# Kernel tuning notes

Hardware: AMD Instinct MI355X
Metric: run time of the kernel (lower is better)

The kernel has to match this reference:

```python
import jax, jax.numpy as jnp
import numpy as np

EPS = 1e-5  # torch LayerNorm default

def ln(x, g, b):
    m = jnp.mean(x, axis=-1, keepdims=True)
    v = jnp.var(x, axis=-1, keepdims=True)
    return (x - m) / jnp.sqrt(v + EPS) * g + b

def setup_inputs() -> dict:
    key = jax.random.key(0)
    H, B, L = 1024, 8, 2048
    ks = jax.random.split(key, 4)
    s = 0.02
    f32 = jnp.float32
    return {
        "x_seq": jax.random.normal(ks[0], (B, L, H), f32),
        "h_prev": jnp.zeros((B, H), f32),
        "w_z": (jax.random.normal(ks[1], (H, 2 * H), f32) * s),
        "b_z": jnp.zeros((H,), f32),
        "w_r": (jax.random.normal(ks[2], (H, 2 * H), f32) * s),
        "b_r": jnp.zeros((H,), f32),
        "w_h": (jax.random.normal(ks[3], (H, 2 * H), f32) * s),
        "b_h": jnp.zeros((H,), f32),
        "g_in": jnp.ones((H,), f32), "b_in": jnp.zeros((H,), f32),
        "g_st": jnp.ones((H,), f32), "b_st": jnp.zeros((H,), f32),
        "g_out": jnp.ones((H,), f32), "b_out": jnp.zeros((H,), f32),
    }

def reference(x_seq, h_prev, w_z, b_z, w_r, b_r, w_h, b_h,
              g_in, b_in, g_st, b_st, g_out, b_out):
    # Dropout is identity (eval mode / p applied only in training).
    H = x_seq.shape[-1]
    xn = ln(x_seq, g_in, b_in)  # [B,L,H]
    # Precompute the input-dependent halves of each Linear([x_t, h]) in one
    # big batched GEMM per gate (math identical to cat+Linear per step).
    gx_z = jnp.einsum('blh,oh->blo', xn, w_z[:, :H]) + b_z
    gx_r = jnp.einsum('blh,oh->blo', xn, w_r[:, :H]) + b_r
    gx_h = jnp.einsum('blh,oh->blo', xn, w_h[:, :H]) + b_h
    wz_h, wr_h, wh_h = w_z[:, H:], w_r[:, H:], w_h[:, H:]

    def step(h, inp):
        gz, gr, gh = inp  # each [B,H]
        hn = ln(h, g_st, b_st)
        z = jax.nn.sigmoid(gz + hn @ wz_h.T)
        r = jax.nn.sigmoid(gr + hn @ wr_h.T)
        h_cand = jnp.tanh(gh + (r * hn) @ wh_h.T)
        h_new = (1.0 - z) * h + z * h_cand
        return h_new, ln(h_new, g_out, b_out)

    # scan over time (leading axis L)
    seq = (jnp.swapaxes(gx_z, 0, 1), jnp.swapaxes(gx_r, 0, 1), jnp.swapaxes(gx_h, 0, 1))
    h_fin, outs = jax.lax.scan(step, h_prev, seq)
    return jnp.swapaxes(outs, 0, 1), h_fin  # [B,L,H], [B,H]
```

## Files before the change

### kernel.cpp

```cpp
#include <hip/hip_runtime.h>
#include <stdint.h>
#include <math.h>

#define HD 1024
#define BB 8
#define LL 2048
#define NBLK 256
#define NTHR 512

typedef unsigned short u16;
typedef unsigned int u32;
typedef unsigned long long u64;

using bf16x8 = __attribute__((ext_vector_type(8))) short;
using f32x4  = __attribute__((ext_vector_type(4))) float;

__device__ __forceinline__ u16 f2bf(float f) {
  u32 x = __float_as_uint(f);
  x += 0x7fffu + ((x >> 16) & 1u);
  return (u16)(x >> 16);
}
__device__ __forceinline__ float bf2f(u16 u) {
  return __uint_as_float(((u32)u) << 16);
}
__device__ __forceinline__ float dot4(float4 a, float4 b) {
  return fmaf(a.x, b.x, fmaf(a.y, b.y, fmaf(a.z, b.z, a.w * b.w)));
}
__device__ __forceinline__ float sigmoidf(float x) { return 1.f / (1.f + expf(-x)); }

__device__ __forceinline__ float2 cload2(const u64* p) {
  u64 v = __hip_atomic_load(p, __ATOMIC_RELAXED, __HIP_MEMORY_SCOPE_AGENT);
  float2 r;
  r.x = __uint_as_float((u32)v);
  r.y = __uint_as_float((u32)(v >> 32));
  return r;
}
__device__ __forceinline__ void cstore1(float* p, float a) {
  __hip_atomic_store((u32*)p, __float_as_uint(a), __ATOMIC_RELAXED, __HIP_MEMORY_SCOPE_AGENT);
}

__device__ __forceinline__ void bar_arrive(u32* bar, int b, int n) {
  int inst = n & 3;
  __hip_atomic_fetch_add(&bar[(b * 4 + inst) * 16], 1u,
                         __ATOMIC_RELAXED, __HIP_MEMORY_SCOPE_AGENT);
}
__device__ __forceinline__ void bar_wait(u32* bar, int b, int n) {
  int inst = n & 3;
  u32 tgt = (u32)((n >> 2) + 1) * 32u;
  while (__hip_atomic_load(&bar[(b * 4 + inst) * 16],
                           __ATOMIC_RELAXED, __HIP_MEMORY_SCOPE_AGENT) < tgt)
    __builtin_amdgcn_s_sleep(1);
}

__global__ __launch_bounds__(256) void k_ln_x(const float* __restrict__ x,
    const float* __restrict__ g, const float* __restrict__ b,
    u16* __restrict__ xn) {
  int row = blockIdx.x;
  int t = threadIdx.x;
  const float4* xr = (const float4*)(x + (size_t)row * HD);
  float4 v = xr[t];
  float s = v.x + v.y + v.z + v.w;
  float ss = v.x * v.x + v.y * v.y + v.z * v.z + v.w * v.w;
#pragma unroll
  for (int off = 32; off; off >>= 1) { s += __shfl_down(s, off); ss += __shfl_down(ss, off); }
  __shared__ float red[8];
  if ((t & 63) == 0) { red[t >> 6] = s; red[4 + (t >> 6)] = ss; }
  __syncthreads();
  s = red[0] + red[1] + red[2] + red[3];
  ss = red[4] + red[5] + red[6] + red[7];
  float m = s * (1.0f / HD);
  float rstd = rsqrtf(ss * (1.0f / HD) - m * m + 1e-5f);
  float4 gv = ((const float4*)g)[t];
  float4 bv = ((const float4*)b)[t];
  ushort4 o;
  o.x = f2bf((v.x - m) * rstd * gv.x + bv.x);
  o.y = f2bf((v.y - m) * rstd * gv.y + bv.y);
  o.z = f2bf((v.z - m) * rstd * gv.z + bv.z);
  o.w = f2bf((v.w - m) * rstd * gv.w + bv.w);
  *(ushort4*)(xn + (size_t)row * HD + t * 4) = o;
}

__global__ __launch_bounds__(256) void k_out_ln(float* __restrict__ y,
    const float* __restrict__ g, const float* __restrict__ b) {
  int row = blockIdx.x;
  int t = threadIdx.x;
  float4* yr = (float4*)(y + (size_t)row * HD);
  float4 v = yr[t];
  float s = v.x + v.y + v.z + v.w;
  float ss = v.x * v.x + v.y * v.y + v.z * v.z + v.w * v.w;
#pragma unroll
  for (int off = 32; off; off >>= 1) { s += __shfl_down(s, off); ss += __shfl_down(ss, off); }
  __shared__ float red[8];
  if ((t & 63) == 0) { red[t >> 6] = s; red[4 + (t >> 6)] = ss; }
  __syncthreads();
  s = red[0] + red[1] + red[2] + red[3];
  ss = red[4] + red[5] + red[6] + red[7];
  float m = s * (1.0f / HD);
  float rstd = rsqrtf(ss * (1.0f / HD) - m * m + 1e-5f);
  float4 gv = ((const float4*)g)[t];
  float4 bv = ((const float4*)b)[t];
  float4 o;
  o.x = (v.x - m) * rstd * gv.x + bv.x;
  o.y = (v.y - m) * rstd * gv.y + bv.y;
  o.z = (v.z - m) * rstd * gv.z + bv.z;
  o.w = (v.w - m) * rstd * gv.w + bv.w;
  yr[t] = o;
}

__global__ __launch_bounds__(256) void k_pack_win(const float* __restrict__ wz,
    const float* __restrict__ wr, const float* __restrict__ wh,
    u16* __restrict__ win) {
  int gid = blockIdx.x;
  int gate = gid >> 10, o = gid & 1023;
  const float* w = (gate == 0) ? wz : ((gate == 1) ? wr : wh);
  const float* row = w + (size_t)o * (2 * HD);
  int t = threadIdx.x;
  float4 a = ((const float4*)row)[t];
  ushort4 ua;
  ua.x = f2bf(a.x); ua.y = f2bf(a.y); ua.z = f2bf(a.z); ua.w = f2bf(a.w);
  *(ushort4*)(win + (size_t)gid * HD + t * 4) = ua;
}

__global__ __launch_bounds__(256) void k_slice_w(const float* __restrict__ wz,
    const float* __restrict__ wr, const float* __restrict__ wh,
    float* __restrict__ Wrec) {
  int gid = blockIdx.x;
  int gate = gid >> 10, o = gid & 1023;
  const float* w = (gate == 0) ? wz : ((gate == 1) ? wr : wh);
  int t = threadIdx.x;
  float4 v = ((const float4*)(w + (size_t)o * (2 * HD) + HD))[t];
  ((float4*)(Wrec + ((size_t)gate << 20) + ((size_t)o << 10)))[t] = v;
}

__global__ __launch_bounds__(256) void k_gemm(const u16* __restrict__ A,
    const u16* __restrict__ Bw, u16* __restrict__ C) {
  __shared__ u16 As[128 * 32];
  __shared__ u16 Bs[128 * 32];
  int tid = threadIdx.x;
  int bx = blockIdx.x % 24;
  int by = blockIdx.x / 24;
  int m0 = by * 128, n0 = bx * 128;
  int lane = tid & 63, wave = tid >> 6;
  int wr = wave >> 1, wc = wave & 1;
  int rl = lane & 15, kq = (lane >> 4) * 8;
  f32x4 acc[4][4] = {};
  int srow = tid >> 2, skb = (tid & 3) * 8;
  for (int k0 = 0; k0 < 1024; k0 += 32) {
    __syncthreads();
#pragma unroll
    for (int i = 0; i < 2; i++) {
      int row = srow + i * 64;
      uint4 av = *(const uint4*)(A + (size_t)(m0 + row) * 1024 + k0 + skb);
      *(uint4*)(As + row * 32 + skb) = av;
      uint4 bv = *(const uint4*)(Bw + (size_t)(n0 + row) * 1024 + k0 + skb);
      *(uint4*)(Bs + row * 32 + skb) = bv;
    }
    __syncthreads();
    bf16x8 af[4], bg[4];
#pragma unroll
    for (int mi = 0; mi < 4; mi++)
      af[mi] = *(const bf16x8*)(As + (wr * 64 + mi * 16 + rl) * 32 + kq);
#pragma unroll
    for (int ni = 0; ni < 4; ni++)
      bg[ni] = *(const bf16x8*)(Bs + (wc * 64 + ni * 16 + rl) * 32 + kq);
#pragma unroll
    for (int mi = 0; mi < 4; mi++)
#pragma unroll
      for (int ni = 0; ni < 4; ni++)
        acc[mi][ni] = __builtin_amdgcn_mfma_f32_16x16x32_bf16(af[mi], bg[ni], acc[mi][ni], 0, 0, 0);
  }
  int rowq = (lane >> 4) * 4;
#pragma unroll
  for (int mi = 0; mi < 4; mi++)
#pragma unroll
    for (int ni = 0; ni < 4; ni++)
#pragma unroll
      for (int r = 0; r < 4; r++) {
        int row = m0 + wr * 64 + mi * 16 + rowq + r;
        int col = n0 + wc * 64 + ni * 16 + rl;
        C[(size_t)row * 3072 + col] = f2bf(acc[mi][ni][r]);
      }
}

__global__ __launch_bounds__(NTHR, 1) void k_rec(
    float* __restrict__ hglob, float* __restrict__ rglob,
    const float* __restrict__ Wrec, const u16* __restrict__ gx,
    const float* __restrict__ bz, const float* __restrict__ br,
    const float* __restrict__ bh, const float* __restrict__ g_st,
    const float* __restrict__ b_st, const float* __restrict__ h0,
    float* __restrict__ out, u32* __restrict__ bar) {
  __shared__ float hn_s[HD];
  __shared__ float u_s[HD];
  __shared__ float2 red2[8];
  const int t = threadIdx.x;
  const int bid = blockIdx.x;
  const int b = bid >> 5, ob = bid & 31;
  const int w8 = t >> 6, ln = t & 63;
  const int q = ln & 3;
  const int o_fin = ob * 32 + w8 * 4 + q;

  const float4* wz4 = (const float4*)(Wrec + (size_t)(ob * 32 + w8 * 4) * HD) + ln * 4;
  const float4* wr4 = wz4 + (1u << 18);
  const float4* wh4 = wz4 + (2u << 18);
  const float biZ = bz[o_fin], biR = br[o_fin], bhc = bh[o_fin];
  const float2 gm2 = ((const float2*)g_st)[t];
  const float2 bt2 = ((const float2*)b_st)[t];
  const u16* gp = gx + ((size_t)b * LL) * 3072 + o_fin;
  float* outp = out + ((size_t)b * LL) * HD + o_fin;
  const u64* hsrc = (const u64*)(hglob + (size_t)b * HD) + t;
  const u64* rsrc = (const u64*)(rglob + (size_t)b * HD) + t;
  float* hpub = hglob + b * HD + o_fin;
  float* rpub = rglob + b * HD + o_fin;

  float ho = h0[b * HD + o_fin];
  u16 gZ = gp[0], gR = gp[1024], gH = gp[2048];
  gp += 3072;

  for (int step = 0; step < LL; step++) {
    float2 h2 = cload2(hsrc);
    float s = h2.x + h2.y;
    float ss = fmaf(h2.x, h2.x, h2.y * h2.y);
#pragma unroll
    for (int mk = 1; mk < 64; mk <<= 1) { s += __shfl_xor(s, mk); ss += __shfl_xor(ss, mk); }
    if (ln == 0) { float2 rv; rv.x = s; rv.y = ss; red2[w8] = rv; }
    __syncthreads();
    s = 0.f; ss = 0.f;
#pragma unroll
    for (int i = 0; i < 8; i++) { float2 rv = red2[i]; s += rv.x; ss += rv.y; }
    float m = s * (1.0f / HD);
    float rstd = rsqrtf(ss * (1.0f / HD) - m * m + 1e-5f);
    float2 hn;
    hn.x = fmaf((h2.x - m) * rstd, gm2.x, bt2.x);
    hn.y = fmaf((h2.y - m) * rstd, gm2.y, bt2.y);
    ((float2*)hn_s)[t] = hn;
    __syncthreads();
    float4 hsl0 = ((const float4*)hn_s)[ln * 4 + 0];
    float4 hsl1 = ((const float4*)hn_s)[ln * 4 + 1];
    float4 hsl2 = ((const float4*)hn_s)[ln * 4 + 2];
    float4 hsl3 = ((const float4*)hn_s)[ln * 4 + 3];
    float a0 = 0.f, a1 = 0.f, a2 = 0.f, a3 = 0.f;
#pragma unroll
    for (int jj = 0; jj < 4; jj++) {
      float4 h4 = (jj == 0) ? hsl0 : ((jj == 1) ? hsl1 : ((jj == 2) ? hsl2 : hsl3));
      a0 += dot4(wr4[jj], h4);
      a1 += dot4(wr4[256 + jj], h4);
      a2 += dot4(wr4[512 + jj], h4);
      a3 += dot4(wr4[768 + jj], h4);
    }
#pragma unroll
    for (int mk = 1; mk < 64; mk <<= 1) {
      a0 += __shfl_xor(a0, mk); a1 += __shfl_xor(a1, mk);
      a2 += __shfl_xor(a2, mk); a3 += __shfl_xor(a3, mk);
    }
    if (ln < 4) {
      float av = (q == 0) ? a0 : ((q == 1) ? a1 : ((q == 2) ? a2 : a3));
      cstore1(rpub, sigmoidf(av + bf2f(gR) + biR));
    }
    __syncthreads();
    if (t == 0) bar_arrive(bar, b, 2 * step);
    a0 = 0.f; a1 = 0.f; a2 = 0.f; a3 = 0.f;
#pragma unroll
    for (int jj = 0; jj < 4; jj++) {
      float4 h4 = (jj == 0) ? hsl0 : ((jj == 1) ? hsl1 : ((jj == 2) ? hsl2 : hsl3));
      a0 += dot4(wz4[jj], h4);
      a1 += dot4(wz4[256 + jj], h4);
      a2 += dot4(wz4[512 + jj], h4);
      a3 += dot4(wz4[768 + jj], h4);
    }
#pragma unroll
    for (int mk = 1; mk < 64; mk <<= 1) {
      a0 += __shfl_xor(a0, mk); a1 += __shfl_xor(a1, mk);
      a2 += __shfl_xor(a2, mk); a3 += __shfl_xor(a3, mk);
    }
    float zv = 0.f;
    if (ln < 4) {
      float av = (q == 0) ? a0 : ((q == 1) ? a1 : ((q == 2) ? a2 : a3));
      zv = sigmoidf(av + bf2f(gZ) + biZ);
    }
    if (t == 0) bar_wait(bar, b, 2 * step);
    __syncthreads();
    float2 rr = cload2(rsrc);
    float2 uu;
    uu.x = rr.x * hn.x;
    uu.y = rr.y * hn.y;
    ((float2*)u_s)[t] = uu;
    __syncthreads();
    a0 = 0.f; a1 = 0.f; a2 = 0.f; a3 = 0.f;
#pragma unroll
    for (int jj = 0; jj < 4; jj++) {
      float4 u4 = ((const float4*)u_s)[ln * 4 + jj];
      a0 += dot4(wh4[jj], u4);
      a1 += dot4(wh4[256 + jj], u4);
      a2 += dot4(wh4[512 + jj], u4);
      a3 += dot4(wh4[768 + jj], u4);
    }
#pragma unroll
    for (int mk = 1; mk < 64; mk <<= 1) {
      a0 += __shfl_xor(a0, mk); a1 += __shfl_xor(a1, mk);
      a2 += __shfl_xor(a2, mk); a3 += __shfl_xor(a3, mk);
    }
    float hnew = 0.f;
    if (ln < 4) {
      float av = (q == 0) ? a0 : ((q == 1) ? a1 : ((q == 2) ? a2 : a3));
      float hc = tanhf(av + bf2f(gH) + bhc);
      hnew = fmaf(zv, hc - ho, ho);
      ho = hnew;
      cstore1(hpub, hnew);
    }
    __syncthreads();
    if (t == 0) bar_arrive(bar, b, 2 * step + 1);
    if (ln < 4) outp[0] = hnew;
    outp += HD;
    gZ = gp[0]; gR = gp[1024]; gH = gp[2048];
    gp += 3072;
    if (t == 0) bar_wait(bar, b, 2 * step + 1);
    __syncthreads();
  }
}

__global__ __launch_bounds__(256) void k_copy(const float* __restrict__ src,
    float* __restrict__ dst, int n4) {
  int i = blockIdx.x * blockDim.x + threadIdx.x;
  if (i < n4) ((float4*)dst)[i] = ((const float4*)src)[i];
}

extern "C" void kernel_launch(void* const* d_in, const int* in_sizes, int n_in,
                              void* d_out, int out_size, void* d_ws, size_t ws_size,
                              hipStream_t stream) {
  (void)in_sizes; (void)n_in; (void)out_size; (void)ws_size;
  const float* x    = (const float*)d_in[0];
  const float* h0   = (const float*)d_in[1];
  const float* wz   = (const float*)d_in[2];
  const float* bz   = (const float*)d_in[3];
  const float* wr   = (const float*)d_in[4];
  const float* br   = (const float*)d_in[5];
  const float* wh   = (const float*)d_in[6];
  const float* bh   = (const float*)d_in[7];
  const float* g_in = (const float*)d_in[8];
  const float* b_in = (const float*)d_in[9];
  const float* g_st = (const float*)d_in[10];
  const float* b_st = (const float*)d_in[11];
  const float* g_out= (const float*)d_in[12];
  const float* b_out= (const float*)d_in[13];
  float* out = (float*)d_out;

  char* ws = (char*)d_ws;
  u16*   xn   = (u16*)(ws);
  float* Wrec = (float*)(ws);
  u16*   win  = (u16*)(ws + 33554432ull);
  u16*   gx   = (u16*)(ws + 39845888ull);
  float* hgl  = (float*)(ws + 140509184ull);
  float* rgl  = (float*)(ws + 140541952ull);
  u32*   bar  = (u32*)(ws + 140574720ull);

  k_pack_win<<<dim3(3072), dim3(256), 0, stream>>>(wz, wr, wh, win);
  k_ln_x<<<dim3(16384), dim3(256), 0, stream>>>(x, g_in, b_in, xn);
  k_gemm<<<dim3(3072), dim3(256), 0, stream>>>(xn, win, gx);
  k_slice_w<<<dim3(3072), dim3(256), 0, stream>>>(wz, wr, wh, Wrec);
  hipMemsetAsync(bar, 0, 4096, stream);
  hipMemcpyAsync(hgl, h0, (size_t)BB * HD * sizeof(float),
                 hipMemcpyDeviceToDevice, stream);
  k_rec<<<dim3(NBLK), dim3(NTHR), 0, stream>>>(hgl, rgl, Wrec, gx, bz, br, bh,
                                               g_st, b_st, h0, out, bar);
  k_out_ln<<<dim3(16384), dim3(256), 0, stream>>>(out, g_out, b_out);
  k_copy<<<dim3(8), dim3(256), 0, stream>>>(hgl, out + (size_t)16384 * 1024, 2048);
}
```

Baseline: 10.87 ms.

## Replace counter barriers with tagged flag-data lines for h and r exchange

Removes the atomic-counter barriers in the recurrent kernel. Each published value now carries its step number as a tag in a 64-bit word, which holds two bf16 values, so consumers spin on the data itself. Double-buffering by step parity avoids overwrite races. Weight access is also re-laid so lanes read contiguous float4s, and each lane computes all four outputs instead of selecting one. This is meant to shorten the per-step critical path of barrier plus reload, at the cost of rounding h and r to bf16 while they are exchanged between blocks.

After: 16.60 ms. 52.7% more time.

```diff
diff --git a/kernel.cpp b/kernel.cpp
--- a/kernel.cpp
+++ b/kernel.cpp
@@ -27,29 +27,31 @@
   return fmaf(a.x, b.x, fmaf(a.y, b.y, fmaf(a.z, b.z, a.w * b.w)));
 }
 __device__ __forceinline__ float sigmoidf(float x) { return 1.f / (1.f + expf(-x)); }
-
-__device__ __forceinline__ float2 cload2(const u64* p) {
+__device__ __forceinline__ float4 unpk4(u64 v) {
+  float4 f;
+  f.x = bf2f((u16)v);
+  f.y = bf2f((u16)(v >> 16));
+  f.z = bf2f((u16)(v >> 32));
+  f.w = bf2f((u16)(v >> 48));
+  return f;
+}
+
+__device__ __forceinline__ float2 poll_line(const u64* p, u32 tag) {
   u64 v = __hip_atomic_load(p, __ATOMIC_RELAXED, __HIP_MEMORY_SCOPE_AGENT);
+  while ((u32)v != tag) {
+    __builtin_amdgcn_s_sleep(1);
+    v = __hip_atomic_load(p, __ATOMIC_RELAXED, __HIP_MEMORY_SCOPE_AGENT);
+  }
+  u32 d = (u32)(v >> 32);
   float2 r;
-  r.x = __uint_as_float((u32)v);
-  r.y = __uint_as_float((u32)(v >> 32));
+  r.x = __uint_as_float((d & 0xffffu) << 16);
+  r.y = __uint_as_float(d & 0xffff0000u);
   return r;
 }
-__device__ __forceinline__ void cstore1(float* p, float a) {
-  __hip_atomic_store((u32*)p, __float_as_uint(a), __ATOMIC_RELAXED, __HIP_MEMORY_SCOPE_AGENT);
-}
-
-__device__ __forceinline__ void bar_arrive(u32* bar, int b, int n) {
-  int inst = n & 3;
-  __hip_atomic_fetch_add(&bar[(b * 4 + inst) * 16], 1u,
-                         __ATOMIC_RELAXED, __HIP_MEMORY_SCOPE_AGENT);
-}
-__device__ __forceinline__ void bar_wait(u32* bar, int b, int n) {
-  int inst = n & 3;
-  u32 tgt = (u32)((n >> 2) + 1) * 32u;
-  while (__hip_atomic_load(&bar[(b * 4 + inst) * 16],
-                           __ATOMIC_RELAXED, __HIP_MEMORY_SCOPE_AGENT) < tgt)
-    __builtin_amdgcn_s_sleep(1);
+__device__ __forceinline__ void pub_line(u64* p, u32 tag, float a, float b) {
+  u32 d = (u32)f2bf(a) | ((u32)f2bf(b) << 16);
+  __hip_atomic_store(p, ((u64)d << 32) | (u64)tag,
+                     __ATOMIC_RELAXED, __HIP_MEMORY_SCOPE_AGENT);
 }
 
 __global__ __launch_bounds__(256) void k_ln_x(const float* __restrict__ x,
@@ -182,13 +184,22 @@
       }
 }
 
+__global__ __launch_bounds__(256) void k_init_hx(const float* __restrict__ h0,
+    u64* __restrict__ hx) {
+  int i = blockIdx.x * 256 + threadIdx.x;
+  int b = i >> 9, line = i & 511;
+  float2 v = ((const float2*)h0)[i];
+  u32 d = (u32)f2bf(v.x) | ((u32)f2bf(v.y) << 16);
+  hx[(size_t)b * 1024 + line] = ((u64)d << 32);
+}
+
 __global__ __launch_bounds__(NTHR, 1) void k_rec(
-    float* __restrict__ hglob, float* __restrict__ rglob,
+    u64* __restrict__ hx, u64* __restrict__ rx,
     const float* __restrict__ Wrec, const u16* __restrict__ gx,
     const float* __restrict__ bz, const float* __restrict__ br,
     const float* __restrict__ bh, const float* __restrict__ g_st,
     const float* __restrict__ b_st, const float* __restrict__ h0,
-    float* __restrict__ out, u32* __restrict__ bar) {
+    float* __restrict__ out, float* __restrict__ hfin) {
   __shared__ float hn_s[HD];
   __shared__ float u_s[HD];
   __shared__ float2 red2[8];
@@ -196,28 +207,28 @@
   const int bid = blockIdx.x;
   const int b = bid >> 5, ob = bid & 31;
   const int w8 = t >> 6, ln = t & 63;
-  const int q = ln & 3;
-  const int o_fin = ob * 32 + w8 * 4 + q;
-
-  const float4* wz4 = (const float4*)(Wrec + (size_t)(ob * 32 + w8 * 4) * HD) + ln * 4;
-  const float4* wr4 = wz4 + (1u << 18);
-  const float4* wh4 = wz4 + (2u << 18);
-  const float biZ = bz[o_fin], biR = br[o_fin], bhc = bh[o_fin];
+  const int o0 = ob * 32 + w8 * 4;
+
+  const float4* wrow = (const float4*)(Wrec + (size_t)o0 * HD);
+  const float4 bz4 = *(const float4*)(bz + o0);
+  const float4 br4 = *(const float4*)(br + o0);
+  const float4 bh4 = *(const float4*)(bh + o0);
   const float2 gm2 = ((const float2*)g_st)[t];
   const float2 bt2 = ((const float2*)b_st)[t];
-  const u16* gp = gx + ((size_t)b * LL) * 3072 + o_fin;
-  float* outp = out + ((size_t)b * LL) * HD + o_fin;
-  const u64* hsrc = (const u64*)(hglob + (size_t)b * HD) + t;
-  const u64* rsrc = (const u64*)(rglob + (size_t)b * HD) + t;
-  float* hpub = hglob + b * HD + o_fin;
-  float* rpub = rglob + b * HD + o_fin;
-
-  float ho = h0[b * HD + o_fin];
-  u16 gZ = gp[0], gR = gp[1024], gH = gp[2048];
-  gp += 3072;
+  const u16* gbase = gx + ((size_t)b * LL) * 3072 + o0;
+  float* outp = out + ((size_t)b * LL) * HD + o0;
+  u64* hx_b = hx + (size_t)b * 1024;
+  u64* rx_b = rx + (size_t)b * 1024;
+  const int publine = ob * 16 + w8 * 2 + (ln & 1);
+
+  float4 hom = *(const float4*)(h0 + b * HD + o0);
+  u64 gz8 = *(const u64*)(gbase);
+  u64 gr8 = *(const u64*)(gbase + 1024);
+  u64 gh8 = *(const u64*)(gbase + 2048);
 
   for (int step = 0; step < LL; step++) {
-    float2 h2 = cload2(hsrc);
+    const int par = step & 1;
+    float2 h2 = poll_line(hx_b + par * 512 + t, (u32)step);
     float s = h2.x + h2.y;
     float ss = fmaf(h2.x, h2.x, h2.y * h2.y);
 #pragma unroll
@@ -234,87 +245,95 @@
     hn.y = fmaf((h2.y - m) * rstd, gm2.y, bt2.y);
     ((float2*)hn_s)[t] = hn;
     __syncthreads();
-    float4 hsl0 = ((const float4*)hn_s)[ln * 4 + 0];
-    float4 hsl1 = ((const float4*)hn_s)[ln * 4 + 1];
-    float4 hsl2 = ((const float4*)hn_s)[ln * 4 + 2];
-    float4 hsl3 = ((const float4*)hn_s)[ln * 4 + 3];
+    float4 hsl[4];
+#pragma unroll
+    for (int jj = 0; jj < 4; jj++) hsl[jj] = ((const float4*)hn_s)[jj * 64 + ln];
     float a0 = 0.f, a1 = 0.f, a2 = 0.f, a3 = 0.f;
 #pragma unroll
     for (int jj = 0; jj < 4; jj++) {
-      float4 h4 = (jj == 0) ? hsl0 : ((jj == 1) ? hsl1 : ((jj == 2) ? hsl2 : hsl3));
-      a0 += dot4(wr4[jj], h4);
-      a1 += dot4(wr4[256 + jj], h4);
-      a2 += dot4(wr4[512 + jj], h4);
-      a3 += dot4(wr4[768 + jj], h4);
+      int idx = (1 << 18) + jj * 64 + ln;
+      a0 += dot4(wrow[idx], hsl[jj]);
+      a1 += dot4(wrow[idx + 256], hsl[jj]);
+      a2 += dot4(wrow[idx + 512], hsl[jj]);
+      a3 += dot4(wrow[idx + 768], hsl[jj]);
     }
 #pragma unroll
     for (int mk = 1; mk < 64; mk <<= 1) {
       a0 += __shfl_xor(a0, mk); a1 += __shfl_xor(a1, mk);
       a2 += __shfl_xor(a2, mk); a3 += __shfl_xor(a3, mk);
     }
-    if (ln < 4) {
-      float av = (q == 0) ? a0 : ((q == 1) ? a1 : ((q == 2) ? a2 : a3));
-      cstore1(rpub, sigmoidf(av + bf2f(gR) + biR));
-    }
-    __syncthreads();
-    if (t == 0) bar_arrive(bar, b, 2 * step);
+    float4 gr4 = unpk4(gr8);
+    float r0 = sigmoidf(a0 + gr4.x + br4.x);
+    float r1 = sigmoidf(a1 + gr4.y + br4.y);
+    float r2v = sigmoidf(a2 + gr4.z + br4.z);
+    float r3v = sigmoidf(a3 + gr4.w + br4.w);
+    if (ln < 2) {
+      float pa = ln ? r2v : r0;
+      float pb = ln ? r3v : r1;
+      pub_line(rx_b + par * 512 + publine, (u32)step, pa, pb);
+    }
     a0 = 0.f; a1 = 0.f; a2 = 0.f; a3 = 0.f;
 #pragma unroll
     for (int jj = 0; jj < 4; jj++) {
-      float4 h4 = (jj == 0) ? hsl0 : ((jj == 1) ? hsl1 : ((jj == 2) ? hsl2 : hsl3));
-      a0 += dot4(wz4[jj], h4);
-      a1 += dot4(wz4[256 + jj], h4);
-      a2 += dot4(wz4[512 + jj], h4);
-      a3 += dot4(wz4[768 + jj], h4);
+      int idx = jj * 64 + ln;
+      a0 += dot4(wrow[idx], hsl[jj]);
+      a1 += dot4(wrow[idx + 256], hsl[jj]);
+      a2 += dot4(wrow[idx + 512], hsl[jj]);
+      a3 += dot4(wrow[idx + 768], hsl[jj]);
     }
 #pragma unroll
     for (int mk = 1; mk < 64; mk <<= 1) {
       a0 += __shfl_xor(a0, mk); a1 += __shfl_xor(a1, mk);
       a2 += __shfl_xor(a2, mk); a3 += __shfl_xor(a3, mk);
     }
-    float zv = 0.f;
-    if (ln < 4) {
-      float av = (q == 0) ? a0 : ((q == 1) ? a1 : ((q == 2) ? a2 : a3));
-      zv = sigmoidf(av + bf2f(gZ) + biZ);
-    }
-    if (t == 0) bar_wait(bar, b, 2 * step);
-    __syncthreads();
-    float2 rr = cload2(rsrc);
-    float2 uu;
-    uu.x = rr.x * hn.x;
-    uu.y = rr.y * hn.y;
-    ((float2*)u_s)[t] = uu;
+    float4 gz4 = unpk4(gz8);
+    float4 zv;
+    zv.x = sigmoidf(a0 + gz4.x + bz4.x);
+    zv.y = sigmoidf(a1 + gz4.y + bz4.y);
+    zv.z = sigmoidf(a2 + gz4.z + bz4.z);
+    zv.w = sigmoidf(a3 + gz4.w + bz4.w);
+    float2 r2 = poll_line(rx_b + par * 512 + t, (u32)step);
+    float2 u2;
+    u2.x = r2.x * hn.x;
+    u2.y = r2.y * hn.y;
+    ((float2*)u_s)[t] = u2;
     __syncthreads();
     a0 = 0.f; a1 = 0.f; a2 = 0.f; a3 = 0.f;
 #pragma unroll
     for (int jj = 0; jj < 4; jj++) {
-      float4 u4 = ((const float4*)u_s)[ln * 4 + jj];
-      a0 += dot4(wh4[jj], u4);
-      a1 += dot4(wh4[256 + jj], u4);
-      a2 += dot4(wh4[512 + jj], u4);
-      a3 += dot4(wh4[768 + jj], u4);
+      float4 u4 = ((const float4*)u_s)[jj * 64 + ln];
+      int idx = (2 << 18) + jj * 64 + ln;
+      a0 += dot4(wrow[idx], u4);
+      a1 += dot4(wrow[idx + 256], u4);
+      a2 += dot4(wrow[idx + 512], u4);
+      a3 += dot4(wrow[idx + 768], u4);
     }
 #pragma unroll
     for (int mk = 1; mk < 64; mk <<= 1) {
       a0 += __shfl_xor(a0, mk); a1 += __shfl_xor(a1, mk);
       a2 += __shfl_xor(a2, mk); a3 += __shfl_xor(a3, mk);
     }
-    float hnew = 0.f;
-    if (ln < 4) {
-      float av = (q == 0) ? a0 : ((q == 1) ? a1 : ((q == 2) ? a2 : a3));
-      float hc = tanhf(av + bf2f(gH) + bhc);
-      hnew = fmaf(zv, hc - ho, ho);
-      ho = hnew;
-      cstore1(hpub, hnew);
-    }
-    __syncthreads();
-    if (t == 0) bar_arrive(bar, b, 2 * step + 1);
-    if (ln < 4) outp[0] = hnew;
+    float4 gh4 = unpk4(gh8);
+    float4 hnew;
+    hnew.x = fmaf(zv.x, tanhf(a0 + gh4.x + bh4.x) - hom.x, hom.x);
+    hnew.y = fmaf(zv.y, tanhf(a1 + gh4.y + bh4.y) - hom.y, hom.y);
+    hnew.z = fmaf(zv.z, tanhf(a2 + gh4.z + bh4.z) - hom.z, hom.z);
+    hnew.w = fmaf(zv.w, tanhf(a3 + gh4.w + bh4.w) - hom.w, hom.w);
+    hom = hnew;
+    if (ln < 2) {
+      float pa = ln ? hnew.z : hnew.x;
+      float pb = ln ? hnew.w : hnew.y;
+      pub_line(hx_b + (par ^ 1) * 512 + publine, (u32)(step + 1), pa, pb);
+    }
+    float hsel = (ln == 0) ? hnew.x : ((ln == 1) ? hnew.y : ((ln == 2) ? hnew.z : hnew.w));
+    if (ln < 4) outp[ln] = hsel;
     outp += HD;
-    gZ = gp[0]; gR = gp[1024]; gH = gp[2048];
-    gp += 3072;
-    if (t == 0) bar_wait(bar, b, 2 * step + 1);
-    __syncthreads();
+    if (step == LL - 1 && ln < 4) hfin[b * HD + o0 + ln] = hsel;
+    int ns = (step + 1 < LL) ? (step + 1) : step;
+    const u16* gn = gbase + (size_t)ns * 3072;
+    gz8 = *(const u64*)(gn);
+    gr8 = *(const u64*)(gn + 1024);
+    gh8 = *(const u64*)(gn + 2048);
   }
 }
 
@@ -349,19 +368,18 @@
   float* Wrec = (float*)(ws);
   u16*   win  = (u16*)(ws + 33554432ull);
   u16*   gx   = (u16*)(ws + 39845888ull);
-  float* hgl  = (float*)(ws + 140509184ull);
-  float* rgl  = (float*)(ws + 140541952ull);
-  u32*   bar  = (u32*)(ws + 140574720ull);
+  u64*   hx   = (u64*)(ws + 140509184ull);
+  u64*   rx   = (u64*)(ws + 140574720ull);
+  float* hfin = (float*)(ws + 140640256ull);
 
   k_pack_win<<<dim3(3072), dim3(256), 0, stream>>>(wz, wr, wh, win);
   k_ln_x<<<dim3(16384), dim3(256), 0, stream>>>(x, g_in, b_in, xn);
   k_gemm<<<dim3(3072), dim3(256), 0, stream>>>(xn, win, gx);
   k_slice_w<<<dim3(3072), dim3(256), 0, stream>>>(wz, wr, wh, Wrec);
-  hipMemsetAsync(bar, 0, 4096, stream);
-  hipMemcpyAsync(hgl, h0, (size_t)BB * HD * sizeof(float),
-                 hipMemcpyDeviceToDevice, stream);
-  k_rec<<<dim3(NBLK), dim3(NTHR), 0, stream>>>(hgl, rgl, Wrec, gx, bz, br, bh,
-                                               g_st, b_st, h0, out, bar);
+  hipMemsetAsync(hx, 0xFF, 131072, stream);
+  k_init_hx<<<dim3(16), dim3(256), 0, stream>>>(h0, hx);
+  k_rec<<<dim3(NBLK), dim3(NTHR), 0, stream>>>(hx, rx, Wrec, gx, bz, br, bh,
+                                               g_st, b_st, h0, out, hfin);
   k_out_ln<<<dim3(16384), dim3(256), 0, stream>>>(out, g_out, b_out);
-  k_copy<<<dim3(8), dim3(256), 0, stream>>>(hgl, out + (size_t)16384 * 1024, 2048);
-}
+  k_copy<<<dim3(8), dim3(256), 0, stream>>>(hfin, out + (size_t)16384 * 1024, 2048);
+}
```
